# Performance work log

Hardware: AMD Instinct MI355X
Metric: run time of the kernel (lower is better)

## Reference

```python
import jax, jax.numpy as jnp
import numpy as np

N_NODES = 1_000_000
FEAT_DIM = 128
EMBED_DIM = 128
BATCH = 8192
NUM_SAMPLE = 10
N_LABELED = 16384
EPS = 1e-6
TEMP = 5.0


def setup_inputs() -> dict:
    key = jax.random.key(0)
    ks = jax.random.split(key, 8)
    return {
        "nodes": jax.random.randint(ks[0], (BATCH,), 0, N_NODES),
        "neigh_idx": jax.random.randint(ks[1], (BATCH, NUM_SAMPLE), 0, N_NODES),
        "pos_index": jax.random.randint(ks[2], (N_LABELED,), 0, N_NODES),
        "neg_index": jax.random.randint(ks[3], (N_LABELED,), 0, N_NODES),
        "features": jax.random.normal(ks[4], (N_NODES, FEAT_DIM), dtype=jnp.float32),
        "weight": jax.random.normal(ks[5], (EMBED_DIM, 2 * FEAT_DIM), dtype=jnp.float32) * (1.0 / np.sqrt(2 * FEAT_DIM)),
        "pos_vector": jax.random.normal(ks[6], (1, FEAT_DIM), dtype=jnp.float32),
        "neg_vector": jax.random.normal(ks[7], (1, FEAT_DIM), dtype=jnp.float32),
    }


def _update_vector(vec, x):
    # torch CosineSimilarity(dim=1, eps=1e-6) between [1,D] vec and [M,D] x -> [M]
    dot = jnp.einsum("md,d->m", x, vec[0])
    nv = jnp.maximum(jnp.linalg.norm(vec[0]), EPS)
    nx = jnp.maximum(jnp.linalg.norm(x, axis=1), EPS)
    cos = dot / (nv * nx)
    w = jax.nn.softmax(cos / TEMP)[None, :]  # softmax_with_temperature, t=5
    return jax.lax.stop_gradient(w @ x)  # [1, D], detached in torch


def reference(nodes, neigh_idx, pos_index, neg_index, features, weight, pos_vector, neg_vector):
    # Mean aggregator over sampled neighbors: [B, S, D] -> [B, D]
    neigh_feats = jnp.mean(features[neigh_idx], axis=1)
    # update_label_vector side computation (running vectors already initialized)
    new_pos = _update_vector(pos_vector, features[pos_index])
    new_neg = _update_vector(neg_vector, features[neg_index])
    # self features gather + concat + weight.mm + relu
    self_feats = features[nodes]                      # [B, D]
    combined = jnp.concatenate([self_feats, neigh_feats], axis=1)  # [B, 2D]
    out = jax.nn.relu(weight @ combined.T)            # [E, B]
    return out, new_pos, new_neg
```

## Files before the change

kernel.cpp:

```cpp
#include <hip/hip_runtime.h>
#include <hip/hip_bf16.h>
#include <stdint.h>

#define BATCH 8192
#define NSAMP 10
#define FDIM 128
#define K2 256
#define EDIM 128
#define NLAB 16384
#define EPSF 1e-6f

#define CPAD 264

typedef __bf16 bf16x8 __attribute__((ext_vector_type(8)));
typedef float f32x4 __attribute__((ext_vector_type(4)));

struct alignas(8) bfx4 { __hip_bfloat16 a, b, c, d; };

#define NPART 2048

__global__ __launch_bounds__(256) void fusedA(
    const int* __restrict__ nodes, const int* __restrict__ neigh,
    const int* __restrict__ pos_idx, const int* __restrict__ neg_idx,
    const float* __restrict__ feats,
    const float* __restrict__ pos_vec, const float* __restrict__ neg_vec,
    const float* __restrict__ W,
    float* __restrict__ partial,
    float* __restrict__ out)
{
    __shared__ __hip_bfloat16 comb[32][CPAD];

    int blk  = blockIdx.x;
    int tid  = threadIdx.x;
    int lane = tid & 63;
    int wv   = tid >> 6;
    int hl   = lane & 31;
    int half = lane >> 5;
    int hw   = wv * 2 + half;

    if (blk < 256) {
        int n0 = blk * 32;

        for (int rr = 0; rr < 4; ++rr) {
            int lr  = hw * 4 + rr;
            int row = n0 + lr;
            int ids[NSAMP + 1];
            ids[0] = nodes[row];
            #pragma unroll
            for (int j = 0; j < NSAMP; ++j) ids[1 + j] = neigh[row * NSAMP + j];

            f32x4 s = ((const f32x4*)(feats + (size_t)ids[0] * FDIM))[hl];
            f32x4 acc = {0.f, 0.f, 0.f, 0.f};
            #pragma unroll
            for (int j = 0; j < NSAMP; ++j) {
                f32x4 v = ((const f32x4*)(feats + (size_t)ids[1 + j] * FDIM))[hl];
                acc += v;
            }
            acc *= 0.1f;

            bfx4 t;
            t.a = __float2bfloat16(s[0]); t.b = __float2bfloat16(s[1]);
            t.c = __float2bfloat16(s[2]); t.d = __float2bfloat16(s[3]);
            *(bfx4*)(&comb[lr][4 * hl]) = t;
            t.a = __float2bfloat16(acc[0]); t.b = __float2bfloat16(acc[1]);
            t.c = __float2bfloat16(acc[2]); t.d = __float2bfloat16(acc[3]);
            *(bfx4*)(&comb[lr][FDIM + 4 * hl]) = t;
        }
        __syncthreads();

        int llo = lane & 15, lhi = lane >> 4;
        int m0 = wv * 32;

        f32x4 acc[2][2];
        #pragma unroll
        for (int i = 0; i < 2; ++i)
            #pragma unroll
            for (int j = 0; j < 2; ++j) { f32x4 z = {0.f,0.f,0.f,0.f}; acc[i][j] = z; }

        #pragma unroll
        for (int k0 = 0; k0 < K2; k0 += 32) {
            bf16x8 a[2], b[2];
            #pragma unroll
            for (int mi = 0; mi < 2; ++mi) {
                const float* wp = W + (size_t)(m0 + 16*mi + llo) * K2 + k0 + lhi*8;
                f32x4 w0 = ((const f32x4*)wp)[0];
                f32x4 w1 = ((const f32x4*)wp)[1];
                bf16x8 af;
                af[0] = (__bf16)w0[0]; af[1] = (__bf16)w0[1];
                af[2] = (__bf16)w0[2]; af[3] = (__bf16)w0[3];
                af[4] = (__bf16)w1[0]; af[5] = (__bf16)w1[1];
                af[6] = (__bf16)w1[2]; af[7] = (__bf16)w1[3];
                a[mi] = af;
            }
            #pragma unroll
            for (int ni = 0; ni < 2; ++ni) {
                const uint4* p = (const uint4*)(&comb[16*ni + llo][k0 + lhi*8]);
                b[ni] = __builtin_bit_cast(bf16x8, *p);
            }
            #pragma unroll
            for (int mi = 0; mi < 2; ++mi)
                #pragma unroll
                for (int ni = 0; ni < 2; ++ni)
                    acc[mi][ni] = __builtin_amdgcn_mfma_f32_16x16x32_bf16(a[mi], b[ni], acc[mi][ni], 0, 0, 0);
        }

        #pragma unroll
        for (int mi = 0; mi < 2; ++mi)
            #pragma unroll
            for (int ni = 0; ni < 2; ++ni)
                #pragma unroll
                for (int j = 0; j < 4; ++j) {
                    int row = m0 + 16*mi + lhi*4 + j;
                    int col = n0 + 16*ni + llo;
                    out[(size_t)row * BATCH + col] = fmaxf(acc[mi][ni][j], 0.f);
                }
    } else {
        int b     = blk - 256;
        int sel   = b >> 9;
        int inner = b & 511;
        int wid   = inner * 4 + wv;
        const int*   idx = sel ? neg_idx : pos_idx;
        const float* vec = sel ? neg_vec : pos_vec;

        f32x4 v4 = ((const f32x4*)vec)[hl];
        float pv = v4[0]*v4[0] + v4[1]*v4[1] + v4[2]*v4[2] + v4[3]*v4[3];
        #pragma unroll
        for (int off = 16; off; off >>= 1) pv += __shfl_xor(pv, off);
        float inv5nv = 1.f / (5.f * fmaxf(sqrtf(pv), EPSF));

        f32x4 a4 = {0.f, 0.f, 0.f, 0.f};
        float es = 0.f;
        int base = wid * 8;
        #pragma unroll
        for (int it = 0; it < 4; ++it) {
            int id = idx[base + 2 * it + half];
            f32x4 x = ((const f32x4*)(feats + (size_t)id * FDIM))[hl];
            float d  = x[0]*v4[0] + x[1]*v4[1] + x[2]*v4[2] + x[3]*v4[3];
            float nx = x[0]*x[0] + x[1]*x[1] + x[2]*x[2] + x[3]*x[3];
            #pragma unroll
            for (int off = 16; off; off >>= 1) {
                d  += __shfl_xor(d, off);
                nx += __shfl_xor(nx, off);
            }
            nx = fmaxf(sqrtf(nx), EPSF);
            float e = __expf(d * inv5nv / nx);
            es += e;
            a4 += e * x;
        }
        #pragma unroll
        for (int c = 0; c < 4; ++c) a4[c] += __shfl_xor(a4[c], 32);
        es += __shfl_xor(es, 32);
        float* pw = partial + ((size_t)sel * NPART + wid) * 132;
        if (lane < 32) ((f32x4*)pw)[lane] = a4;
        if (lane == 0) pw[128] = es;
    }
}

__global__ __launch_bounds__(256) void stage2k(
    const float* __restrict__ partial, float* __restrict__ outv)
{
    int lane = threadIdx.x & 63;
    int wv   = threadIdx.x >> 6;
    int widx = blockIdx.x * 4 + wv;
    int sel = widx >> 7;
    int d   = widx & 127;
    const float* p = partial + (size_t)sel * NPART * 132;
    float s = 0.f, es = 0.f;
    for (int w = lane; w < NPART; w += 64) {
        s  += p[w * 132 + d];
        es += p[w * 132 + 128];
    }
    #pragma unroll
    for (int off = 32; off; off >>= 1) {
        s  += __shfl_xor(s, off);
        es += __shfl_xor(es, off);
    }
    if (lane == 0) outv[sel * 128 + d] = s / es;
}

extern "C" void kernel_launch(void* const* d_in, const int* in_sizes, int n_in,
                              void* d_out, int out_size, void* d_ws, size_t ws_size,
                              hipStream_t stream) {
    const int*   nodes = (const int*)d_in[0];
    const int*   neigh = (const int*)d_in[1];
    const int*   pos_i = (const int*)d_in[2];
    const int*   neg_i = (const int*)d_in[3];
    const float* feats = (const float*)d_in[4];
    const float* W     = (const float*)d_in[5];
    const float* pvec  = (const float*)d_in[6];
    const float* nvec  = (const float*)d_in[7];
    float* out = (float*)d_out;

    float* partial = (float*)d_ws;

    hipLaunchKernelGGL(fusedA, dim3(1280), dim3(256), 0, stream,
                       nodes, neigh, pos_i, neg_i, feats, pvec, nvec, W, partial, out);
    hipLaunchKernelGGL(stage2k, dim3(64), dim3(256), 0, stream,
                       partial, out + 1048576);
}
```

Baseline: 33.22 us.

## Fuse final softmax reduction into main kernel via last-block atomic counter

Measured after the change: 79.25 us. +138.6%, slower.

```diff
diff --git a/kernel.cpp b/kernel.cpp
--- a/kernel.cpp
+++ b/kernel.cpp
@@ -11,13 +11,13 @@
 #define EPSF 1e-6f
 
 #define CPAD 264
+#define NPB 512
+#define PARTIAL_BYTES (2 * NPB * 132 * 4)
 
 typedef __bf16 bf16x8 __attribute__((ext_vector_type(8)));
 typedef float f32x4 __attribute__((ext_vector_type(4)));
 
 struct alignas(8) bfx4 { __hip_bfloat16 a, b, c, d; };
-
-#define NPART 2048
 
 __global__ __launch_bounds__(256) void fusedA(
     const int* __restrict__ nodes, const int* __restrict__ neigh,
@@ -26,9 +26,12 @@
     const float* __restrict__ pos_vec, const float* __restrict__ neg_vec,
     const float* __restrict__ W,
     float* __restrict__ partial,
+    unsigned* __restrict__ cnt,
     float* __restrict__ out)
 {
     __shared__ __hip_bfloat16 comb[32][CPAD];
+    __shared__ float red[4][132];
+    __shared__ int lastFlag;
 
     int blk  = blockIdx.x;
     int tid  = threadIdx.x;
@@ -41,6 +44,7 @@
     if (blk < 256) {
         int n0 = blk * 32;
 
+        #pragma unroll 2
         for (int rr = 0; rr < 4; ++rr) {
             int lr  = hw * 4 + rr;
             int row = n0 + lr;
@@ -70,6 +74,7 @@
 
         int llo = lane & 15, lhi = lane >> 4;
         int m0 = wv * 32;
+        int n0b = blk * 32;
 
         f32x4 acc[2][2];
         #pragma unroll
@@ -111,7 +116,7 @@
                 #pragma unroll
                 for (int j = 0; j < 4; ++j) {
                     int row = m0 + 16*mi + lhi*4 + j;
-                    int col = n0 + 16*ni + llo;
+                    int col = n0b + 16*ni + llo;
                     out[(size_t)row * BATCH + col] = fmaxf(acc[mi][ni][j], 0.f);
                 }
     } else {
@@ -150,32 +155,34 @@
         #pragma unroll
         for (int c = 0; c < 4; ++c) a4[c] += __shfl_xor(a4[c], 32);
         es += __shfl_xor(es, 32);
-        float* pw = partial + ((size_t)sel * NPART + wid) * 132;
-        if (lane < 32) ((f32x4*)pw)[lane] = a4;
-        if (lane == 0) pw[128] = es;
+
+        if (lane < 32) *(f32x4*)(&red[wv][4 * hl]) = a4;
+        if (lane == 0) red[wv][128] = es;
+        __syncthreads();
+        if (tid < 132) {
+            float s = red[0][tid] + red[1][tid] + red[2][tid] + red[3][tid];
+            partial[((size_t)sel * NPB + inner) * 132 + tid] = s;
+        }
+        __syncthreads();
+
+        if (tid == 0) {
+            __threadfence();
+            unsigned old = atomicAdd(cnt, 1u);
+            lastFlag = (old == 2u * NPB - 1u);
+        }
+        __syncthreads();
+        if (lastFlag) {
+            __threadfence();
+            int sel2 = tid >> 7, d = tid & 127;
+            const float* p = partial + (size_t)sel2 * NPB * 132;
+            float s = 0.f, es2 = 0.f;
+            for (int w = 0; w < NPB; ++w) {
+                s   += p[w * 132 + d];
+                es2 += p[w * 132 + 128];
+            }
+            out[1048576 + sel2 * 128 + d] = s / es2;
+        }
     }
-}
-
-__global__ __launch_bounds__(256) void stage2k(
-    const float* __restrict__ partial, float* __restrict__ outv)
-{
-    int lane = threadIdx.x & 63;
-    int wv   = threadIdx.x >> 6;
-    int widx = blockIdx.x * 4 + wv;
-    int sel = widx >> 7;
-    int d   = widx & 127;
-    const float* p = partial + (size_t)sel * NPART * 132;
-    float s = 0.f, es = 0.f;
-    for (int w = lane; w < NPART; w += 64) {
-        s  += p[w * 132 + d];
-        es += p[w * 132 + 128];
-    }
-    #pragma unroll
-    for (int off = 32; off; off >>= 1) {
-        s  += __shfl_xor(s, off);
-        es += __shfl_xor(es, off);
-    }
-    if (lane == 0) outv[sel * 128 + d] = s / es;
 }
 
 extern "C" void kernel_launch(void* const* d_in, const int* in_sizes, int n_in,
@@ -191,10 +198,11 @@
     const float* nvec  = (const float*)d_in[7];
     float* out = (float*)d_out;
 
-    float* partial = (float*)d_ws;
-
+    float*    partial = (float*)d_ws;
+    unsigned* cnt     = (unsigned*)((char*)d_ws + PARTIAL_BYTES);
+
+    hipMemsetAsync(cnt, 0, 4, stream);
     hipLaunchKernelGGL(fusedA, dim3(1280), dim3(256), 0, stream,
-                       nodes, neigh, pos_i, neg_i, feats, pvec, nvec, W, partial, out);
-    hipLaunchKernelGGL(stage2k, dim3(64), dim3(256), 0, stream,
-                       partial, out + 1048576);
+                       nodes, neigh, pos_i, neg_i, feats, pvec, nvec, W,
+                       partial, cnt, out);
 }
```
